# Optimization experiments

Measured on AMD Instinct MI355X. Metric: run time of the kernel, lower is better.

Reference implementation:

```python
import jax, jax.numpy as jnp
import numpy as np

D_MODEL = 768
NUM_HEADS = 12
HEAD_DIM = D_MODEL // NUM_HEADS


def setup_inputs() -> dict:
    key = jax.random.key(0)
    ks = jax.random.split(key, 12)
    B, S = 4, 1024
    x = jax.random.normal(ks[0], (B, S, D_MODEL), dtype=jnp.float32)
    boxes = jax.random.uniform(ks[1], (B, S, 4), dtype=jnp.float32)
    s = 1.0 / np.sqrt(D_MODEL)
    Wq = jax.random.normal(ks[2], (D_MODEL, D_MODEL), dtype=jnp.float32) * s
    bq = jnp.zeros((D_MODEL,), dtype=jnp.float32)
    Wk = jax.random.normal(ks[3], (D_MODEL, D_MODEL), dtype=jnp.float32) * s
    bk = jnp.zeros((D_MODEL,), dtype=jnp.float32)
    Wv = jax.random.normal(ks[4], (D_MODEL, D_MODEL), dtype=jnp.float32) * s
    bv = jnp.zeros((D_MODEL,), dtype=jnp.float32)
    Wo = jax.random.normal(ks[5], (D_MODEL, D_MODEL), dtype=jnp.float32) * s
    bo = jnp.zeros((D_MODEL,), dtype=jnp.float32)
    spatial_bias = jax.random.normal(ks[6], (NUM_HEADS,), dtype=jnp.float32)
    return {"x": x, "boxes": boxes, "Wq": Wq, "bq": bq, "Wk": Wk, "bk": bk,
            "Wv": Wv, "bv": bv, "Wo": Wo, "bo": bo, "spatial_bias": spatial_bias}


def reference(x, boxes, Wq, bq, Wk, bk, Wv, bv, Wo, bo, spatial_bias):
    B, S, _ = x.shape
    H, Dh = NUM_HEADS, HEAD_DIM
    # projections -> [B, H, S, Dh]
    def proj(W, b):
        return (x @ W.T + b).reshape(B, S, H, Dh).transpose(0, 2, 1, 3)
    Q, K, V = proj(Wq, bq), proj(Wk, bk), proj(Wv, bv)
    scores = jnp.einsum('bhsd,bhtd->bhst', Q, K) / np.sqrt(Dh)
    # spatial bias from box-center pairwise distances
    centers = jnp.stack([(boxes[:, :, 0] + boxes[:, :, 2]) * 0.5,
                         (boxes[:, :, 1] + boxes[:, :, 3]) * 0.5], axis=-1)  # [B,S,2]
    diff = centers[:, :, None, :] - centers[:, None, :, :]                    # [B,S,S,2]
    dist = jnp.linalg.norm(diff, axis=-1)                                     # [B,S,S]
    bias = -dist[:, None, :, :] * spatial_bias[None, :, None, None]           # [B,H,S,S]
    attn = jax.nn.softmax(scores + bias, axis=-1)
    attended = jnp.einsum('bhst,bhtd->bhsd', attn, V)
    attended = attended.transpose(0, 2, 1, 3).reshape(B, S, H * Dh)
    return attended @ Wo.T + bo
```

## Files before the change

kernel.cpp:

```cpp
#include <hip/hip_runtime.h>
#include <stdint.h>

#define NHEADS 12
#define HDIM   64
#define NB     4
#define SQ     1024
#define DM     768
#define NROWS  (NB*SQ)
#define NWE    (DM*DM)
#define NXE    (NROWS*DM)

typedef __attribute__((ext_vector_type(8))) short short8;
typedef __attribute__((ext_vector_type(4))) float f32x4;

__device__ __forceinline__ unsigned short f2bf(float f) {
  union { float f; unsigned u; } v; v.f = f;
  return (unsigned short)((v.u + 0x7fffu + ((v.u >> 16) & 1u)) >> 16);
}

__device__ __forceinline__ unsigned pack2bf(float lo, float hi) {
  return (unsigned)f2bf(lo) | ((unsigned)f2bf(hi) << 16);
}

__device__ __forceinline__ void gload16(const void* g, void* l) {
  __builtin_amdgcn_global_load_lds((__attribute__((address_space(1))) void*)(void*)g,
                                   (__attribute__((address_space(3))) void*)l, 16, 0, 0);
}

__device__ __forceinline__ void drain_dma() {
  asm volatile("s_waitcnt vmcnt(0)" ::: "memory");
  __builtin_amdgcn_sched_barrier(0);
}

__global__ __launch_bounds__(256) void prep_kernel(
    const float* __restrict__ x, const float* __restrict__ Wq, const float* __restrict__ Wk,
    const float* __restrict__ Wv, const float* __restrict__ Wo, const float* __restrict__ boxes,
    unsigned short* __restrict__ xb, unsigned short* __restrict__ wcat,
    unsigned short* __restrict__ wob, float2* __restrict__ centers) {
  int i = blockIdx.x * 256 + threadIdx.x;
  if (i < NXE) { xb[i] = f2bf(x[i]); return; }
  i -= NXE;
  if (i < NWE) {
    wcat[i]           = f2bf(Wq[i]);
    wcat[NWE + i]     = f2bf(Wk[i]);
    wcat[2 * NWE + i] = f2bf(Wv[i]);
    wob[i]            = f2bf(Wo[i]);
    return;
  }
  i -= NWE;
  if (i < NROWS) {
    float4 bx = ((const float4*)boxes)[i];
    centers[i] = make_float2((bx.x + bx.z) * 0.5f, (bx.y + bx.w) * 0.5f);
  }
}

template <int EPI, int BM, int BN>
__global__ __launch_bounds__(256, 2) void gemm_bt(
    const unsigned short* __restrict__ A, const unsigned short* __restrict__ Bw,
    int K, int tiles_n,
    const float* __restrict__ b0, const float* __restrict__ b1, const float* __restrict__ b2,
    unsigned short* __restrict__ outQ, unsigned short* __restrict__ outK,
    unsigned short* __restrict__ outVt, float* __restrict__ outF) {
  constexpr int MF = BM / 32, NF = BN / 32;
  __shared__ unsigned short lA[2][BM * 32];
  __shared__ unsigned short lB[2][BN * 32];
  const int tid = threadIdx.x, wave = tid >> 6, lane = tid & 63;
  const int tm = blockIdx.x / tiles_n, tn = blockIdx.x % tiles_n;
  const int wr = wave >> 1, wc = wave & 1;
  const int g = lane >> 4, c16 = lane & 15, kb8 = g * 8;

  f32x4 acc[MF][NF];
#pragma unroll
  for (int m = 0; m < MF; m++)
#pragma unroll
    for (int n = 0; n < NF; n++) acc[m][n] = (f32x4){0.f, 0.f, 0.f, 0.f};

  const unsigned short* Abase = A + (size_t)tm * BM * K;
  const unsigned short* Bbase = Bw + (size_t)tn * BN * K;
  const int srow = lane >> 2, scb = (lane & 3) << 4;

  auto stage = [&](int kt, int s) {
#pragma unroll
    for (int c = wave; c < BM / 16; c += 4)
      gload16((const char*)(Abase + (size_t)(c * 16 + srow) * K + kt) + scb,
              (char*)lA[s] + c * 1024);
#pragma unroll
    for (int c = wave; c < BN / 16; c += 4)
      gload16((const char*)(Bbase + (size_t)(c * 16 + srow) * K + kt) + scb,
              (char*)lB[s] + c * 1024);
  };

  stage(0, 0);
  const int nk = K >> 5;
#pragma unroll 1
  for (int i = 0; i < nk; i++) {
    drain_dma();
    __syncthreads();
    if (i + 1 < nk) stage((i + 1) * 32, (i + 1) & 1);
    const unsigned short* sA = lA[i & 1];
    const unsigned short* sB = lB[i & 1];
    short8 a[MF], b[NF];
#pragma unroll
    for (int m = 0; m < MF; m++)
      a[m] = *(const short8*)&sA[(wr * (BM / 2) + m * 16 + c16) * 32 + kb8];
#pragma unroll
    for (int n = 0; n < NF; n++)
      b[n] = *(const short8*)&sB[(wc * (BN / 2) + n * 16 + c16) * 32 + kb8];
#pragma unroll
    for (int m = 0; m < MF; m++)
#pragma unroll
      for (int n = 0; n < NF; n++)
        acc[m][n] = __builtin_amdgcn_mfma_f32_16x16x32_bf16(a[m], b[n], acc[m][n], 0, 0, 0);
  }

#pragma unroll
  for (int m = 0; m < MF; m++) {
    const int gm0 = tm * BM + wr * (BM / 2) + m * 16 + g * 4;
    const int bb = gm0 >> 10, ss0 = gm0 & 1023;
#pragma unroll
    for (int n = 0; n < NF; n++) {
      const int gn = tn * BN + wc * (BN / 2) + n * 16 + c16;
      if (EPI == 0) {
        const int which = gn / DM, nn = gn - which * DM;
        const int h = nn >> 6, dh = nn & 63;
        const float bias = (which == 0 ? b0 : which == 1 ? b1 : b2)[nn];
        const float scale = (which == 0) ? 0.1803368801f : 1.0f;
        if (which == 2) {
          ushort4 pk;
          pk.x = f2bf(acc[m][n][0] + bias);
          pk.y = f2bf(acc[m][n][1] + bias);
          pk.z = f2bf(acc[m][n][2] + bias);
          pk.w = f2bf(acc[m][n][3] + bias);
          *(ushort4*)&outVt[(((size_t)bb * NHEADS + h) * HDIM + dh) * SQ + ss0] = pk;
        } else {
          unsigned short* dst = (which == 0 ? outQ : outK) + ((size_t)bb * NHEADS + h) * SQ * HDIM;
#pragma unroll
          for (int r = 0; r < 4; r++)
            dst[(size_t)(ss0 + r) * HDIM + dh] = f2bf((acc[m][n][r] + bias) * scale);
        }
      } else {
        const float bias = b0[gn];
#pragma unroll
        for (int r = 0; r < 4; r++)
          outF[(size_t)(gm0 + r) * DM + gn] = acc[m][n][r] + bias;
      }
    }
  }
}

#define KVB  64
#define PSTR 72
__global__ __launch_bounds__(256, 3) void attn_kernel(
    const unsigned short* __restrict__ Qb, const unsigned short* __restrict__ Kb,
    const unsigned short* __restrict__ Vt, const float2* __restrict__ centers,
    const float* __restrict__ sbias, unsigned short* __restrict__ attb) {
  __shared__ unsigned short lK[2][KVB * HDIM];
  __shared__ unsigned short lV[2][HDIM * KVB];
  __shared__ float2 lcent[2][KVB];
  __shared__ unsigned short plds[4][16 * PSTR];
  const int tid = threadIdx.x, wave = tid >> 6, lane = tid & 63;
  const int g = lane >> 4, c16 = lane & 15, kb8 = g * 8;
  const int bid = blockIdx.x;
  const int xcd = bid & 7, li = bid >> 3;
  const int bh = xcd * 6 + (li >> 4);
  const int qt = li & 15;
  const int b = bh / NHEADS, h = bh - b * NHEADS;
  const float sb = sbias[h] * 1.44269504f;

  const unsigned short* Qh = Qb + (size_t)bh * SQ * HDIM;
  const char* Kc = (const char*)(Kb + (size_t)bh * SQ * HDIM);
  const char* Vc = (const char*)(Vt + (size_t)bh * HDIM * SQ);
  const float2* cent_g = centers + b * SQ;

  const int l8 = lane >> 3, l7 = lane & 7;
  const int swizL = (l7 * 16) ^ (l8 << 4);

  auto stage = [&](int tbn, int s) {
    const char* kbase = Kc + (size_t)tbn * 128;
#pragma unroll
    for (int j = 0; j < 2; j++) {
      const int i = wave * 2 + j;
      gload16(kbase + i * 1024 + l8 * 128 + swizL, (char*)lK[s] + i * 1024);
    }
    const char* vbase = Vc + (size_t)tbn * 2;
#pragma unroll
    for (int j = 0; j < 2; j++) {
      const int i = wave * 2 + j;
      gload16(vbase + (size_t)(i * 8 + l8) * 2048 + swizL, (char*)lV[s] + i * 1024);
    }
    if (tid < KVB) lcent[s][tid] = cent_g[tbn + tid];
  };

  const int q = qt * 64 + wave * 16 + c16;
  short8 qf[2];
  qf[0] = *(const short8*)&Qh[(size_t)q * HDIM + kb8];
  qf[1] = *(const short8*)&Qh[(size_t)q * HDIM + 32 + kb8];
  const float2 cq = cent_g[q];

  float mreg = -1e30f, lreg = 0.f;
  f32x4 oacc[4];
#pragma unroll
  for (int dd = 0; dd < 4; dd++) oacc[dd] = (f32x4){0.f, 0.f, 0.f, 0.f};

  stage(0, 0);

  const int swk = (c16 & 7) << 4;
#pragma unroll 1
  for (int t = 0; t < SQ / KVB; t++) {
    const int cur = t & 1;
    drain_dma();
    __syncthreads();
    if (t + 1 < SQ / KVB) stage((t + 1) * KVB, cur ^ 1);
    f32x4 sv[4];
#pragma unroll
    for (int cc = 0; cc < 4; cc++) {
      const int rb = (cc * 16 + c16) * 128;
      short8 k0 = *(const short8*)((const char*)lK[cur] + rb + ((g * 16) ^ swk));
      short8 k1 = *(const short8*)((const char*)lK[cur] + rb + ((64 + g * 16) ^ swk));
      f32x4 s = (f32x4){0.f, 0.f, 0.f, 0.f};
      s = __builtin_amdgcn_mfma_f32_16x16x32_bf16(k0, qf[0], s, 0, 0, 0);
      s = __builtin_amdgcn_mfma_f32_16x16x32_bf16(k1, qf[1], s, 0, 0, 0);
      sv[cc] = s;
    }
#pragma unroll
    for (int cc = 0; cc < 4; cc++) {
      const float4* cp = (const float4*)&lcent[cur][cc * 16 + g * 4];
      float4 c01 = cp[0], c23 = cp[1];
      float dx, dy;
      dx = cq.x - c01.x; dy = cq.y - c01.y;
      sv[cc][0] -= __builtin_amdgcn_sqrtf(dx * dx + dy * dy) * sb;
      dx = cq.x - c01.z; dy = cq.y - c01.w;
      sv[cc][1] -= __builtin_amdgcn_sqrtf(dx * dx + dy * dy) * sb;
      dx = cq.x - c23.x; dy = cq.y - c23.y;
      sv[cc][2] -= __builtin_amdgcn_sqrtf(dx * dx + dy * dy) * sb;
      dx = cq.x - c23.z; dy = cq.y - c23.w;
      sv[cc][3] -= __builtin_amdgcn_sqrtf(dx * dx + dy * dy) * sb;
    }
    float lm = -1e30f;
#pragma unroll
    for (int cc = 0; cc < 4; cc++) {
      float a0 = fmaxf(sv[cc][0], sv[cc][1]), a1 = fmaxf(sv[cc][2], sv[cc][3]);
      lm = fmaxf(lm, fmaxf(a0, a1));
    }
    if (!__all(lm <= mreg + 8.0f)) {
      float vmax = fmaxf(lm, __shfl_xor(lm, 16));
      vmax = fmaxf(vmax, __shfl_xor(vmax, 32));
      const float mn = fmaxf(mreg, vmax);
      const float sc = __builtin_amdgcn_exp2f(mreg - mn);
      lreg *= sc;
#pragma unroll
      for (int dd = 0; dd < 4; dd++)
#pragma unroll
        for (int r = 0; r < 4; r++) oacc[dd][r] *= sc;
      mreg = mn;
    }
    float ps = 0.f;
#pragma unroll
    for (int cc = 0; cc < 4; cc++)
#pragma unroll
      for (int r = 0; r < 4; r++) {
        sv[cc][r] = __builtin_amdgcn_exp2f(sv[cc][r] - mreg);
        ps += sv[cc][r];
      }
    lreg += ps;
#pragma unroll
    for (int cc = 0; cc < 4; cc++) {
      uint2 u;
      u.x = pack2bf(sv[cc][0], sv[cc][1]);
      u.y = pack2bf(sv[cc][2], sv[cc][3]);
      *(uint2*)&plds[wave][c16 * PSTR + cc * 16 + g * 4] = u;
    }
#pragma unroll
    for (int kc = 0; kc < 2; kc++) {
      short8 pf = *(const short8*)&plds[wave][c16 * PSTR + kc * 32 + kb8];
#pragma unroll
      for (int dd = 0; dd < 4; dd++) {
        short8 vf = *(const short8*)((const char*)lV[cur] + (dd * 16 + c16) * 128 +
                                     ((kc * 64 + g * 16) ^ swk));
        oacc[dd] = __builtin_amdgcn_mfma_f32_16x16x32_bf16(vf, pf, oacc[dd], 0, 0, 0);
      }
    }
  }
  lreg += __shfl_xor(lreg, 16);
  lreg += __shfl_xor(lreg, 32);
  const float inv = 1.f / lreg;
#pragma unroll
  for (int dd = 0; dd < 4; dd++) {
    uint2 u;
    u.x = pack2bf(oacc[dd][0] * inv, oacc[dd][1] * inv);
    u.y = pack2bf(oacc[dd][2] * inv, oacc[dd][3] * inv);
    *(uint2*)&attb[(size_t)(b * SQ + q) * DM + h * HDIM + dd * 16 + g * 4] = u;
  }
}

extern "C" void kernel_launch(void* const* d_in, const int* in_sizes, int n_in,
                              void* d_out, int out_size, void* d_ws, size_t ws_size,
                              hipStream_t stream) {
  const float* x     = (const float*)d_in[0];
  const float* boxes = (const float*)d_in[1];
  const float* Wq    = (const float*)d_in[2];
  const float* bq    = (const float*)d_in[3];
  const float* Wk    = (const float*)d_in[4];
  const float* bk    = (const float*)d_in[5];
  const float* Wv    = (const float*)d_in[6];
  const float* bv    = (const float*)d_in[7];
  const float* Wo    = (const float*)d_in[8];
  const float* bo    = (const float*)d_in[9];
  const float* sb    = (const float*)d_in[10];

  char* ws = (char*)d_ws;
  unsigned short* xb   = (unsigned short*)(ws);
  unsigned short* wcat = (unsigned short*)(ws + 6291456);
  unsigned short* wob  = (unsigned short*)(ws + 9830400);
  unsigned short* qb   = (unsigned short*)(ws + 11010048);
  unsigned short* kb   = (unsigned short*)(ws + 17301504);
  unsigned short* vtb  = (unsigned short*)(ws + 23592960);
  unsigned short* attb = (unsigned short*)(ws + 29884416);
  float2* centers      = (float2*)(ws + 36175872);
  float* out = (float*)d_out;

  prep_kernel<<<14608, 256, 0, stream>>>(x, Wq, Wk, Wv, Wo, boxes, xb, wcat, wob, centers);
  gemm_bt<0, 128, 128><<<32 * 18, 256, 0, stream>>>(xb, wcat, DM, 18, bq, bk, bv,
                                                    qb, kb, vtb, nullptr);
  attn_kernel<<<768, 256, 0, stream>>>(qb, kb, vtb, centers, sb, attb);
  gemm_bt<1, 64, 64><<<64 * 12, 256, 0, stream>>>(attb, wob, DM, 12, bo, nullptr, nullptr,
                                                  nullptr, nullptr, nullptr, out);
}
```

Baseline: 93.76 us.

## Triple-buffer attention K/V tiles with smaller KV blocks and preloaded centers

The attention kernel now uses 32-key tiles with a three-stage LDS ring. It waits on vmcnt(2) instead of fully draining the DMA each iteration, so two tiles are in flight at once. All box centers for the batch are loaded into LDS once at the start instead of per tile. K, V and P are stored in an MFMA-friendly layout in place of the XOR swizzle. This aims to hide global load latency better, at the cost of more loop iterations and barriers and possible LDS bank conflicts without the swizzle.

```diff
diff --git a/kernel.cpp b/kernel.cpp
--- a/kernel.cpp
+++ b/kernel.cpp
@@ -148,16 +148,16 @@
   }
 }
 
-#define KVB  64
-#define PSTR 72
+#define KVB 32
+#define NT  (SQ / KVB)
 __global__ __launch_bounds__(256, 3) void attn_kernel(
     const unsigned short* __restrict__ Qb, const unsigned short* __restrict__ Kb,
     const unsigned short* __restrict__ Vt, const float2* __restrict__ centers,
     const float* __restrict__ sbias, unsigned short* __restrict__ attb) {
-  __shared__ unsigned short lK[2][KVB * HDIM];
-  __shared__ unsigned short lV[2][HDIM * KVB];
-  __shared__ float2 lcent[2][KVB];
-  __shared__ unsigned short plds[4][16 * PSTR];
+  __shared__ unsigned short lK[3][KVB * HDIM];
+  __shared__ unsigned short lV[3][HDIM * KVB];
+  __shared__ float2 cent_s[SQ];
+  __shared__ unsigned short plds[4][16 * KVB];
   const int tid = threadIdx.x, wave = tid >> 6, lane = tid & 63;
   const int g = lane >> 4, c16 = lane & 15, kb8 = g * 8;
   const int bid = blockIdx.x;
@@ -170,32 +170,22 @@
   const unsigned short* Qh = Qb + (size_t)bh * SQ * HDIM;
   const char* Kc = (const char*)(Kb + (size_t)bh * SQ * HDIM);
   const char* Vc = (const char*)(Vt + (size_t)bh * HDIM * SQ);
-  const float2* cent_g = centers + b * SQ;
-
-  const int l8 = lane >> 3, l7 = lane & 7;
-  const int swizL = (l7 * 16) ^ (l8 << 4);
+
+  for (int i = tid; i < SQ; i += 256) cent_s[i] = centers[b * SQ + i];
+  __syncthreads();
 
   auto stage = [&](int tbn, int s) {
-    const char* kbase = Kc + (size_t)tbn * 128;
-#pragma unroll
-    for (int j = 0; j < 2; j++) {
-      const int i = wave * 2 + j;
-      gload16(kbase + i * 1024 + l8 * 128 + swizL, (char*)lK[s] + i * 1024);
-    }
-    const char* vbase = Vc + (size_t)tbn * 2;
-#pragma unroll
-    for (int j = 0; j < 2; j++) {
-      const int i = wave * 2 + j;
-      gload16(vbase + (size_t)(i * 8 + l8) * 2048 + swizL, (char*)lV[s] + i * 1024);
-    }
-    if (tid < KVB) lcent[s][tid] = cent_g[tbn + tid];
+    gload16(Kc + (size_t)(tbn + (lane & 31)) * 128 + (2 * wave + (lane >> 5)) * 16,
+            (char*)lK[s] + wave * 1024);
+    gload16(Vc + (size_t)lane * 2048 + (size_t)(tbn + wave * 8) * 2,
+            (char*)lV[s] + wave * 1024);
   };
 
   const int q = qt * 64 + wave * 16 + c16;
   short8 qf[2];
   qf[0] = *(const short8*)&Qh[(size_t)q * HDIM + kb8];
   qf[1] = *(const short8*)&Qh[(size_t)q * HDIM + 32 + kb8];
-  const float2 cq = cent_g[q];
+  const float2 cq = cent_s[q];
 
   float mreg = -1e30f, lreg = 0.f;
   f32x4 oacc[4];
@@ -203,28 +193,32 @@
   for (int dd = 0; dd < 4; dd++) oacc[dd] = (f32x4){0.f, 0.f, 0.f, 0.f};
 
   stage(0, 0);
-
-  const int swk = (c16 & 7) << 4;
+  stage(KVB, 1);
+  int cur = 0;
 #pragma unroll 1
-  for (int t = 0; t < SQ / KVB; t++) {
-    const int cur = t & 1;
-    drain_dma();
-    __syncthreads();
-    if (t + 1 < SQ / KVB) stage((t + 1) * KVB, cur ^ 1);
-    f32x4 sv[4];
-#pragma unroll
-    for (int cc = 0; cc < 4; cc++) {
-      const int rb = (cc * 16 + c16) * 128;
-      short8 k0 = *(const short8*)((const char*)lK[cur] + rb + ((g * 16) ^ swk));
-      short8 k1 = *(const short8*)((const char*)lK[cur] + rb + ((64 + g * 16) ^ swk));
+  for (int t = 0; t < NT; t++) {
+    if (t < NT - 1) asm volatile("s_waitcnt vmcnt(2)" ::: "memory");
+    else            asm volatile("s_waitcnt vmcnt(0)" ::: "memory");
+    __builtin_amdgcn_sched_barrier(0);
+    __builtin_amdgcn_s_barrier();
+    if (t + 2 < NT) stage((t + 2) * KVB, (cur + 2) % 3);
+    __builtin_amdgcn_sched_barrier(0);
+    const char* K0 = (const char*)lK[cur];
+    const char* V0 = (const char*)lV[cur];
+    f32x4 sv[2];
+#pragma unroll
+    for (int cc = 0; cc < 2; cc++) {
+      short8 k0 = *(const short8*)(K0 + (size_t)((g * 32) + cc * 16 + c16) * 16);
+      short8 k1 = *(const short8*)(K0 + (size_t)(((4 + g) * 32) + cc * 16 + c16) * 16);
       f32x4 s = (f32x4){0.f, 0.f, 0.f, 0.f};
       s = __builtin_amdgcn_mfma_f32_16x16x32_bf16(k0, qf[0], s, 0, 0, 0);
       s = __builtin_amdgcn_mfma_f32_16x16x32_bf16(k1, qf[1], s, 0, 0, 0);
       sv[cc] = s;
     }
-#pragma unroll
-    for (int cc = 0; cc < 4; cc++) {
-      const float4* cp = (const float4*)&lcent[cur][cc * 16 + g * 4];
+    const int tb = t * KVB;
+#pragma unroll
+    for (int cc = 0; cc < 2; cc++) {
+      const float4* cp = (const float4*)&cent_s[tb + cc * 16 + g * 4];
       float4 c01 = cp[0], c23 = cp[1];
       float dx, dy;
       dx = cq.x - c01.x; dy = cq.y - c01.y;
@@ -236,12 +230,8 @@
       dx = cq.x - c23.z; dy = cq.y - c23.w;
       sv[cc][3] -= __builtin_amdgcn_sqrtf(dx * dx + dy * dy) * sb;
     }
-    float lm = -1e30f;
-#pragma unroll
-    for (int cc = 0; cc < 4; cc++) {
-      float a0 = fmaxf(sv[cc][0], sv[cc][1]), a1 = fmaxf(sv[cc][2], sv[cc][3]);
-      lm = fmaxf(lm, fmaxf(a0, a1));
-    }
+    float lm = fmaxf(fmaxf(fmaxf(sv[0][0], sv[0][1]), fmaxf(sv[0][2], sv[0][3])),
+                     fmaxf(fmaxf(sv[1][0], sv[1][1]), fmaxf(sv[1][2], sv[1][3])));
     if (!__all(lm <= mreg + 8.0f)) {
       float vmax = fmaxf(lm, __shfl_xor(lm, 16));
       vmax = fmaxf(vmax, __shfl_xor(vmax, 32));
@@ -256,30 +246,28 @@
     }
     float ps = 0.f;
 #pragma unroll
-    for (int cc = 0; cc < 4; cc++)
+    for (int cc = 0; cc < 2; cc++)
 #pragma unroll
       for (int r = 0; r < 4; r++) {
         sv[cc][r] = __builtin_amdgcn_exp2f(sv[cc][r] - mreg);
         ps += sv[cc][r];
       }
     lreg += ps;
-#pragma unroll
-    for (int cc = 0; cc < 4; cc++) {
+    char* P0 = (char*)plds + wave * 1024;
+#pragma unroll
+    for (int cc = 0; cc < 2; cc++) {
       uint2 u;
       u.x = pack2bf(sv[cc][0], sv[cc][1]);
       u.y = pack2bf(sv[cc][2], sv[cc][3]);
-      *(uint2*)&plds[wave][c16 * PSTR + cc * 16 + g * 4] = u;
-    }
-#pragma unroll
-    for (int kc = 0; kc < 2; kc++) {
-      short8 pf = *(const short8*)&plds[wave][c16 * PSTR + kc * 32 + kb8];
-#pragma unroll
-      for (int dd = 0; dd < 4; dd++) {
-        short8 vf = *(const short8*)((const char*)lV[cur] + (dd * 16 + c16) * 128 +
-                                     ((kc * 64 + g * 16) ^ swk));
-        oacc[dd] = __builtin_amdgcn_mfma_f32_16x16x32_bf16(vf, pf, oacc[dd], 0, 0, 0);
-      }
-    }
+      *(uint2*)(P0 + (2 * cc + (g >> 1)) * 256 + c16 * 16 + (g & 1) * 8) = u;
+    }
+    short8 pf = *(const short8*)(P0 + (g * 16 + c16) * 16);
+#pragma unroll
+    for (int dd = 0; dd < 4; dd++) {
+      short8 vf = *(const short8*)(V0 + (size_t)(g * 64 + dd * 16 + c16) * 16);
+      oacc[dd] = __builtin_amdgcn_mfma_f32_16x16x32_bf16(vf, pf, oacc[dd], 0, 0, 0);
+    }
+    cur = (cur == 2) ? 0 : cur + 1;
   }
   lreg += __shfl_xor(lreg, 16);
   lreg += __shfl_xor(lreg, 32);
```

Result: slower. 101.5 us (+8.3%).

## Precompute pairwise box distances in prep kernel and change attention LDS layout

Applied to the files above, without the earlier changes.

Adds a pass in the prep kernel that writes the full negative pairwise center-distance matrix (B*S*S floats) to workspace when the workspace is large enough. The attention kernel then reads it with strided global loads instead of computing sqrt per score from centers. It also removes the XOR swizzle on the K/V/P LDS tiles in favour of a column-chunked layout, and switches bf16 packing to the HIP intrinsic. This trades per-score ALU work for about 16MB of extra global writes plus strided reads across all 12 heads, and the unswizzled layout may change bank conflicts.

```diff
diff --git a/kernel.cpp b/kernel.cpp
--- a/kernel.cpp
+++ b/kernel.cpp
@@ -1,4 +1,5 @@
 #include <hip/hip_runtime.h>
+#include <hip/hip_bf16.h>
 #include <stdint.h>
 
 #define NHEADS 12
@@ -9,6 +10,7 @@
 #define NROWS  (NB*SQ)
 #define NWE    (DM*DM)
 #define NXE    (NROWS*DM)
+#define NDIST  (NB*SQ*SQ)
 
 typedef __attribute__((ext_vector_type(8))) short short8;
 typedef __attribute__((ext_vector_type(4))) float f32x4;
@@ -18,8 +20,11 @@
   return (unsigned short)((v.u + 0x7fffu + ((v.u >> 16) & 1u)) >> 16);
 }
 
-__device__ __forceinline__ unsigned pack2bf(float lo, float hi) {
-  return (unsigned)f2bf(lo) | ((unsigned)f2bf(hi) << 16);
+__device__ __forceinline__ unsigned pkbf(float lo, float hi) {
+  __hip_bfloat162 h;
+  h.x = __float2bfloat16(lo);
+  h.y = __float2bfloat16(hi);
+  return *reinterpret_cast<unsigned*>(&h);
 }
 
 __device__ __forceinline__ void gload16(const void* g, void* l) {
@@ -36,7 +41,8 @@
     const float* __restrict__ x, const float* __restrict__ Wq, const float* __restrict__ Wk,
     const float* __restrict__ Wv, const float* __restrict__ Wo, const float* __restrict__ boxes,
     unsigned short* __restrict__ xb, unsigned short* __restrict__ wcat,
-    unsigned short* __restrict__ wob, float2* __restrict__ centers) {
+    unsigned short* __restrict__ wob, float2* __restrict__ centers,
+    float* __restrict__ distb, int ndist) {
   int i = blockIdx.x * 256 + threadIdx.x;
   if (i < NXE) { xb[i] = f2bf(x[i]); return; }
   i -= NXE;
@@ -51,6 +57,16 @@
   if (i < NROWS) {
     float4 bx = ((const float4*)boxes)[i];
     centers[i] = make_float2((bx.x + bx.z) * 0.5f, (bx.y + bx.w) * 0.5f);
+    return;
+  }
+  i -= NROWS;
+  if (i < ndist) {
+    const int q = i & (SQ - 1), t = (i >> 10) & (SQ - 1), b = i >> 20;
+    float4 bt = ((const float4*)boxes)[b * SQ + t];
+    float4 bq = ((const float4*)boxes)[b * SQ + q];
+    float dx = (bt.x + bt.z - bq.x - bq.z) * 0.5f;
+    float dy = (bt.y + bt.w - bq.y - bq.w) * 0.5f;
+    distb[i] = -__builtin_amdgcn_sqrtf(dx * dx + dy * dy);
   }
 }
 
@@ -148,16 +164,18 @@
   }
 }
 
-#define KVB  64
-#define PSTR 72
+#define KVB 64
+#define NT  (SQ / KVB)
+template <bool DIST>
 __global__ __launch_bounds__(256, 3) void attn_kernel(
     const unsigned short* __restrict__ Qb, const unsigned short* __restrict__ Kb,
     const unsigned short* __restrict__ Vt, const float2* __restrict__ centers,
-    const float* __restrict__ sbias, unsigned short* __restrict__ attb) {
+    const float* __restrict__ distb, const float* __restrict__ sbias,
+    unsigned short* __restrict__ attb) {
   __shared__ unsigned short lK[2][KVB * HDIM];
   __shared__ unsigned short lV[2][HDIM * KVB];
-  __shared__ float2 lcent[2][KVB];
-  __shared__ unsigned short plds[4][16 * PSTR];
+  __shared__ unsigned short plds[4][16 * KVB];
+  __shared__ float2 cent_s[DIST ? 1 : SQ];
   const int tid = threadIdx.x, wave = tid >> 6, lane = tid & 63;
   const int g = lane >> 4, c16 = lane & 15, kb8 = g * 8;
   const int bid = blockIdx.x;
@@ -170,32 +188,28 @@
   const unsigned short* Qh = Qb + (size_t)bh * SQ * HDIM;
   const char* Kc = (const char*)(Kb + (size_t)bh * SQ * HDIM);
   const char* Vc = (const char*)(Vt + (size_t)bh * HDIM * SQ);
-  const float2* cent_g = centers + b * SQ;
-
-  const int l8 = lane >> 3, l7 = lane & 7;
-  const int swizL = (l7 * 16) ^ (l8 << 4);
+
+  if (!DIST) {
+    for (int i = tid; i < SQ; i += 256) cent_s[i] = centers[b * SQ + i];
+    __syncthreads();
+  }
 
   auto stage = [&](int tbn, int s) {
-    const char* kbase = Kc + (size_t)tbn * 128;
 #pragma unroll
     for (int j = 0; j < 2; j++) {
-      const int i = wave * 2 + j;
-      gload16(kbase + i * 1024 + l8 * 128 + swizL, (char*)lK[s] + i * 1024);
-    }
-    const char* vbase = Vc + (size_t)tbn * 2;
-#pragma unroll
-    for (int j = 0; j < 2; j++) {
-      const int i = wave * 2 + j;
-      gload16(vbase + (size_t)(i * 8 + l8) * 2048 + swizL, (char*)lV[s] + i * 1024);
-    }
-    if (tid < KVB) lcent[s][tid] = cent_g[tbn + tid];
+      const int c = wave * 2 + j;
+      gload16(Kc + (size_t)(tbn + lane) * 128 + c * 16, (char*)lK[s] + c * 1024);
+      gload16(Vc + (size_t)lane * 2048 + (size_t)(tbn + c * 8) * 2, (char*)lV[s] + c * 1024);
+    }
   };
 
   const int q = qt * 64 + wave * 16 + c16;
   short8 qf[2];
   qf[0] = *(const short8*)&Qh[(size_t)q * HDIM + kb8];
   qf[1] = *(const short8*)&Qh[(size_t)q * HDIM + 32 + kb8];
-  const float2 cq = cent_g[q];
+  float2 cq = make_float2(0.f, 0.f);
+  if (!DIST) cq = cent_s[q];
+  const float* dqg = DIST ? (distb + ((size_t)b * SQ + g * 4) * SQ + q) : nullptr;
 
   float mreg = -1e30f, lreg = 0.f;
   f32x4 oacc[4];
@@ -203,38 +217,47 @@
   for (int dd = 0; dd < 4; dd++) oacc[dd] = (f32x4){0.f, 0.f, 0.f, 0.f};
 
   stage(0, 0);
-
-  const int swk = (c16 & 7) << 4;
 #pragma unroll 1
-  for (int t = 0; t < SQ / KVB; t++) {
+  for (int t = 0; t < NT; t++) {
     const int cur = t & 1;
     drain_dma();
     __syncthreads();
-    if (t + 1 < SQ / KVB) stage((t + 1) * KVB, cur ^ 1);
+    if (t + 1 < NT) stage((t + 1) * KVB, cur ^ 1);
+    const char* K0 = (const char*)lK[cur];
+    const char* V0 = (const char*)lV[cur];
+    const int tb = t * KVB;
     f32x4 sv[4];
 #pragma unroll
     for (int cc = 0; cc < 4; cc++) {
-      const int rb = (cc * 16 + c16) * 128;
-      short8 k0 = *(const short8*)((const char*)lK[cur] + rb + ((g * 16) ^ swk));
-      short8 k1 = *(const short8*)((const char*)lK[cur] + rb + ((64 + g * 16) ^ swk));
+      short8 k0 = *(const short8*)(K0 + g * 1024 + (cc * 16 + c16) * 16);
+      short8 k1 = *(const short8*)(K0 + (4 + g) * 1024 + (cc * 16 + c16) * 16);
       f32x4 s = (f32x4){0.f, 0.f, 0.f, 0.f};
       s = __builtin_amdgcn_mfma_f32_16x16x32_bf16(k0, qf[0], s, 0, 0, 0);
       s = __builtin_amdgcn_mfma_f32_16x16x32_bf16(k1, qf[1], s, 0, 0, 0);
       sv[cc] = s;
     }
-#pragma unroll
-    for (int cc = 0; cc < 4; cc++) {
-      const float4* cp = (const float4*)&lcent[cur][cc * 16 + g * 4];
-      float4 c01 = cp[0], c23 = cp[1];
-      float dx, dy;
-      dx = cq.x - c01.x; dy = cq.y - c01.y;
-      sv[cc][0] -= __builtin_amdgcn_sqrtf(dx * dx + dy * dy) * sb;
-      dx = cq.x - c01.z; dy = cq.y - c01.w;
-      sv[cc][1] -= __builtin_amdgcn_sqrtf(dx * dx + dy * dy) * sb;
-      dx = cq.x - c23.x; dy = cq.y - c23.y;
-      sv[cc][2] -= __builtin_amdgcn_sqrtf(dx * dx + dy * dy) * sb;
-      dx = cq.x - c23.z; dy = cq.y - c23.w;
-      sv[cc][3] -= __builtin_amdgcn_sqrtf(dx * dx + dy * dy) * sb;
+    if (DIST) {
+      const float* dqi = dqg + (size_t)tb * SQ;
+#pragma unroll
+      for (int cc = 0; cc < 4; cc++)
+#pragma unroll
+        for (int r = 0; r < 4; r++)
+          sv[cc][r] = fmaf(dqi[(size_t)(cc * 16 + r) * SQ], sb, sv[cc][r]);
+    } else {
+#pragma unroll
+      for (int cc = 0; cc < 4; cc++) {
+        const float4* cp = (const float4*)&cent_s[tb + cc * 16 + g * 4];
+        float4 c01 = cp[0], c23 = cp[1];
+        float dx, dy;
+        dx = cq.x - c01.x; dy = cq.y - c01.y;
+        sv[cc][0] -= __builtin_amdgcn_sqrtf(dx * dx + dy * dy) * sb;
+        dx = cq.x - c01.z; dy = cq.y - c01.w;
+        sv[cc][1] -= __builtin_amdgcn_sqrtf(dx * dx + dy * dy) * sb;
+        dx = cq.x - c23.x; dy = cq.y - c23.y;
+        sv[cc][2] -= __builtin_amdgcn_sqrtf(dx * dx + dy * dy) * sb;
+        dx = cq.x - c23.z; dy = cq.y - c23.w;
+        sv[cc][3] -= __builtin_amdgcn_sqrtf(dx * dx + dy * dy) * sb;
+      }
     }
     float lm = -1e30f;
 #pragma unroll
@@ -263,20 +286,20 @@
         ps += sv[cc][r];
       }
     lreg += ps;
+    char* P0 = (char*)&plds[wave][0];
 #pragma unroll
     for (int cc = 0; cc < 4; cc++) {
       uint2 u;
-      u.x = pack2bf(sv[cc][0], sv[cc][1]);
-      u.y = pack2bf(sv[cc][2], sv[cc][3]);
-      *(uint2*)&plds[wave][c16 * PSTR + cc * 16 + g * 4] = u;
+      u.x = pkbf(sv[cc][0], sv[cc][1]);
+      u.y = pkbf(sv[cc][2], sv[cc][3]);
+      *(uint2*)(P0 + (cc * 2 + (g >> 1)) * 256 + c16 * 16 + (g & 1) * 8) = u;
     }
 #pragma unroll
     for (int kc = 0; kc < 2; kc++) {
-      short8 pf = *(const short8*)&plds[wave][c16 * PSTR + kc * 32 + kb8];
+      short8 pf = *(const short8*)(P0 + (kc * 4 + g) * 256 + c16 * 16);
 #pragma unroll
       for (int dd = 0; dd < 4; dd++) {
-        short8 vf = *(const short8*)((const char*)lV[cur] + (dd * 16 + c16) * 128 +
-                                     ((kc * 64 + g * 16) ^ swk));
+        short8 vf = *(const short8*)(V0 + (kc * 4 + g) * 1024 + (dd * 16 + c16) * 16);
         oacc[dd] = __builtin_amdgcn_mfma_f32_16x16x32_bf16(vf, pf, oacc[dd], 0, 0, 0);
       }
     }
@@ -287,8 +310,8 @@
 #pragma unroll
   for (int dd = 0; dd < 4; dd++) {
     uint2 u;
-    u.x = pack2bf(oacc[dd][0] * inv, oacc[dd][1] * inv);
-    u.y = pack2bf(oacc[dd][2] * inv, oacc[dd][3] * inv);
+    u.x = pkbf(oacc[dd][0] * inv, oacc[dd][1] * inv);
+    u.y = pkbf(oacc[dd][2] * inv, oacc[dd][3] * inv);
     *(uint2*)&attb[(size_t)(b * SQ + q) * DM + h * HDIM + dd * 16 + g * 4] = u;
   }
 }
@@ -317,12 +340,21 @@
   unsigned short* vtb  = (unsigned short*)(ws + 23592960);
   unsigned short* attb = (unsigned short*)(ws + 29884416);
   float2* centers      = (float2*)(ws + 36175872);
+  float* distb         = (float*)(ws + 36208640);
   float* out = (float*)d_out;
 
-  prep_kernel<<<14608, 256, 0, stream>>>(x, Wq, Wk, Wv, Wo, boxes, xb, wcat, wob, centers);
+  const bool useDist = (ws_size >= 36208640u + (size_t)NDIST * 4u);
+  const int ndist = useDist ? NDIST : 0;
+  const int prep_blocks = (NXE + NWE + NROWS + ndist + 255) / 256;
+
+  prep_kernel<<<prep_blocks, 256, 0, stream>>>(x, Wq, Wk, Wv, Wo, boxes, xb, wcat, wob,
+                                               centers, distb, ndist);
   gemm_bt<0, 128, 128><<<32 * 18, 256, 0, stream>>>(xb, wcat, DM, 18, bq, bk, bv,
                                                     qb, kb, vtb, nullptr);
-  attn_kernel<<<768, 256, 0, stream>>>(qb, kb, vtb, centers, sb, attb);
+  if (useDist)
+    attn_kernel<true><<<768, 256, 0, stream>>>(qb, kb, vtb, centers, distb, sb, attb);
+  else
+    attn_kernel<false><<<768, 256, 0, stream>>>(qb, kb, vtb, centers, distb, sb, attb);
   gemm_bt<1, 64, 64><<<64 * 12, 256, 0, stream>>>(attb, wob, DM, 12, bo, nullptr, nullptr,
                                                   nullptr, nullptr, nullptr, out);
 }
```

Result: slower. 106.8 us (+13.9%).
